# Optimization experiments

Measured on AMD Instinct MI355X. Metric: run time of the kernel, lower is better.

## Reference

```python
import jax, jax.numpy as jnp
import numpy as np
import math

NUM_HEADS = 16
HEAD_DIM = 128
ROPE_BASE = 10000.0


def setup_inputs() -> dict:
    key = jax.random.key(0)
    ks = jax.random.split(key, 6)
    B, S, H = 2, 2048, 2048
    hidden_states = jax.random.normal(ks[0], (B, S, H), dtype=jnp.float32) * 0.02
    # causal additive mask, shape (B, 1, S, S)
    neg = jnp.finfo(jnp.float32).min
    causal = jnp.where(jnp.tril(jnp.ones((S, S), dtype=bool)), 0.0, neg).astype(jnp.float32)
    attention_mask = jnp.broadcast_to(causal[None, None], (B, 1, S, S))
    position_ids = jnp.broadcast_to(jnp.arange(S, dtype=jnp.int64)[None], (B, S))
    scale = 1.0 / math.sqrt(H)
    Wq = jax.random.normal(ks[1], (H, H), dtype=jnp.float32) * scale
    Wk = jax.random.normal(ks[2], (H, H), dtype=jnp.float32) * scale
    Wv = jax.random.normal(ks[3], (H, H), dtype=jnp.float32) * scale
    Wo = jax.random.normal(ks[4], (H, H), dtype=jnp.float32) * scale
    return {"hidden_states": hidden_states, "attention_mask": attention_mask,
            "position_ids": position_ids, "Wq": Wq, "Wk": Wk, "Wv": Wv, "Wo": Wo}


def _rotate_half(x):
    x1, x2 = jnp.split(x, 2, axis=-1)
    return jnp.concatenate((-x2, x1), axis=-1)


def reference(hidden_states, attention_mask, position_ids, Wq, Wk, Wv, Wo):
    B, S, H = hidden_states.shape
    nh, hd = NUM_HEADS, HEAD_DIM

    def shape_heads(x):  # (B,S,H) -> (B,nh,S,hd)
        return x.reshape(B, S, nh, hd).transpose(0, 2, 1, 3)

    q = shape_heads(hidden_states @ Wq.T)
    k = shape_heads(hidden_states @ Wk.T)
    v = shape_heads(hidden_states @ Wv.T)

    kv_seq_len = S  # no past_key_value
    # rotary table: (kv_seq_len, hd)
    inv_freq = 1.0 / (ROPE_BASE ** (jnp.arange(0, hd, 2, dtype=jnp.float32) / hd))
    t = jnp.arange(kv_seq_len, dtype=jnp.float32)
    freqs = jnp.einsum('i,j->ij', t, inv_freq)
    emb = jnp.concatenate((freqs, freqs), axis=-1)
    # gather-based RoPE == table lookup at position_ids: (B,S,hd) -> (B,1,S,hd)
    cos = jnp.cos(emb)[position_ids][:, None]
    sin = jnp.sin(emb)[position_ids][:, None]

    q = q * cos + _rotate_half(q) * sin
    k = k * cos + _rotate_half(k) * sin

    scores = jnp.einsum('bhqd,bhkd->bhqk', q, k) / math.sqrt(hd)
    scores = scores + attention_mask
    scores = jnp.maximum(scores, jnp.finfo(scores.dtype).min)
    probs = jax.nn.softmax(scores.astype(jnp.float32), axis=-1).astype(q.dtype)
    attn = jnp.einsum('bhqk,bhkd->bhqd', probs, v)  # (B,nh,S,hd)
    attn = attn.transpose(0, 2, 1, 3).reshape(B, S, H)
    return attn @ Wo.T
```

## Files before the change

kernel.cpp:

```cpp
#include <hip/hip_runtime.h>
#include <hip/hip_bf16.h>
#include <cstdint>

#define SQ    2048
#define HDIM  2048
#define NH    16
#define HD    128
#define BATCH 2
#define MTOK  (BATCH*SQ)

typedef unsigned short u16;
typedef unsigned int   u32;
typedef __bf16 bf16x8 __attribute__((ext_vector_type(8)));
typedef float  f32x4  __attribute__((ext_vector_type(4)));
typedef float  f32x16 __attribute__((ext_vector_type(16)));
typedef unsigned short u16x4 __attribute__((ext_vector_type(4)));
typedef unsigned int   u32x4 __attribute__((ext_vector_type(4)));

__device__ __forceinline__ u16 f2b(float f) {
  union { float f; unsigned u; } v; v.f = f;
  return (u16)((v.u + 0x7fffu + ((v.u >> 16) & 1u)) >> 16);
}
__device__ __forceinline__ float b2f(u16 b) {
  union { unsigned u; float f; } v; v.u = ((unsigned)b) << 16;
  return v.f;
}

#define GLD_LDS16(gp, lp) __builtin_amdgcn_global_load_lds( \
    (const __attribute__((address_space(1))) uint32_t*)(gp), \
    (__attribute__((address_space(3))) uint32_t*)(lp), 16, 0, 0)

__device__ __forceinline__ f32x16 zero16() {
  f32x16 v;
#pragma unroll
  for (int i = 0; i < 16; ++i) v[i] = 0.f;
  return v;
}

__global__ __launch_bounds__(256) void conv_bf16(const float* __restrict__ in,
                                                 u16* __restrict__ out, int n4) {
  int i = blockIdx.x * 256 + threadIdx.x;
  if (i >= n4) return;
  float4 v = ((const float4*)in)[i];
  u16x4 o;
  o.x = f2b(v.x); o.y = f2b(v.y); o.z = f2b(v.z); o.w = f2b(v.w);
  *(u16x4*)(out + (size_t)i * 4) = o;
}

__global__ void rope_table_k(float* __restrict__ ct, float* __restrict__ st) {
  int s = blockIdx.x, j = threadIdx.x;
  float invf = expf(-(float)j * (9.210340371976184f / 64.0f));
  float ang = (float)s * invf;
  ct[s * 64 + j] = cosf(ang);
  st[s * 64 + j] = sinf(ang);
}

__global__ __launch_bounds__(256) void rope_apply(u16* __restrict__ X,
                                                  const float* __restrict__ ct,
                                                  const float* __restrict__ st) {
  int idx = blockIdx.x * 256 + threadIdx.x;
  int j = idx & 63;
  int row = idx >> 6;
  int s = row & (SQ - 1);
  size_t base = (size_t)row * HD;
  float x1 = b2f(X[base + j]), x2 = b2f(X[base + j + 64]);
  float c = ct[s * 64 + j], sn = st[s * 64 + j];
  X[base + j]      = f2b(x1 * c - x2 * sn);
  X[base + j + 64] = f2b(x2 * c + x1 * sn);
}

template<int MODE>
__global__ __launch_bounds__(256)
void gemm_bt(const u16* __restrict__ A, const u16* __restrict__ Bw,
             void* __restrict__ Cout) {
  __shared__ u16 As[128 * 64];
  __shared__ u16 Bs[128 * 64];
  const int tid = threadIdx.x;
  const int lane = tid & 63;
  const int w = tid >> 6;
  const int m0 = blockIdx.y * 128;
  const int n0 = blockIdx.x * 128;
  const int wm = (w >> 1) * 64;
  const int wn = (w & 1) * 64;
  const int lr = lane >> 3, lc = lane & 7;

  f32x4 zero = {0.f, 0.f, 0.f, 0.f};
  f32x4 acc[4][4];
  for (int i = 0; i < 4; ++i)
    for (int j = 0; j < 4; ++j) acc[i][j] = zero;

  for (int k0 = 0; k0 < HDIM; k0 += 64) {
    __syncthreads();
#pragma unroll
    for (int j = 0; j < 4; ++j) {
      int r = (w * 4 + j) * 8 + lr;
      GLD_LDS16(A  + (size_t)(m0 + r) * HDIM + k0 + lc * 8, &As[(w * 4 + j) * 512]);
      GLD_LDS16(Bw + (size_t)(n0 + r) * HDIM + k0 + lc * 8, &Bs[(w * 4 + j) * 512]);
    }
    __syncthreads();
#pragma unroll
    for (int kk = 0; kk < 2; ++kk) {
      int ko = kk * 32 + (lane >> 4) * 8;
      bf16x8 a[4], b[4];
#pragma unroll
      for (int i = 0; i < 4; ++i)
        a[i] = *(const bf16x8*)&As[(wm + i * 16 + (lane & 15)) * 64 + ko];
#pragma unroll
      for (int i = 0; i < 4; ++i)
        b[i] = *(const bf16x8*)&Bs[(wn + i * 16 + (lane & 15)) * 64 + ko];
#pragma unroll
      for (int mi = 0; mi < 4; ++mi)
#pragma unroll
        for (int ni = 0; ni < 4; ++ni)
          acc[mi][ni] = __builtin_amdgcn_mfma_f32_16x16x32_bf16(
              a[mi], b[ni], acc[mi][ni], 0, 0, 0);
    }
  }

  const int cl = lane & 15, rg = (lane >> 4) * 4;
#pragma unroll
  for (int mi = 0; mi < 4; ++mi) {
#pragma unroll
    for (int ni = 0; ni < 4; ++ni) {
      int mbase = m0 + wm + mi * 16 + rg;
      int n = n0 + wn + ni * 16 + cl;
      if (MODE == 2) {
        float* O = (float*)Cout;
#pragma unroll
        for (int r = 0; r < 4; ++r)
          O[(size_t)(mbase + r) * HDIM + n] = acc[mi][ni][r];
      } else if (MODE == 0) {
        u16* O = (u16*)Cout;
        int h = n >> 7, d = n & 127;
#pragma unroll
        for (int r = 0; r < 4; ++r) {
          int m = mbase + r;
          int b = m >> 11, s = m & (SQ - 1);
          O[((size_t)(b * NH + h) * SQ + s) * HD + d] = f2b(acc[mi][ni][r]);
        }
      } else {
        u16* O = (u16*)Cout;
        int h = n >> 7, d = n & 127;
        int b = mbase >> 11, s = mbase & (SQ - 1);
        u16x4 pk;
        pk.x = f2b(acc[mi][ni][0]); pk.y = f2b(acc[mi][ni][1]);
        pk.z = f2b(acc[mi][ni][2]); pk.w = f2b(acc[mi][ni][3]);
        *(u16x4*)&O[((size_t)(b * NH + h) * HD + d) * SQ + s] = pk;
      }
    }
  }
}


__device__ __forceinline__ void stage_kv(u16* ksb, u16* vsb,
                                         const u16* __restrict__ Kg,
                                         const u16* __restrict__ Vg,
                                         int kv0, int w, int lane) {
#pragma unroll
  for (int i = 0; i < 4; ++i) {
    int chunk = (w * 4 + i) * 64 + lane;
    int row = chunk >> 4, c16 = chunk & 15;
    int csrc = c16 ^ (row & 7);
    GLD_LDS16(Kg + (size_t)(kv0 + row) * HD + csrc * 8, ksb + (w * 4 + i) * 512);
  }
#pragma unroll
  for (int i = 0; i < 4; ++i) {
    int chunk = (w * 4 + i) * 64 + lane;
    int d = chunk >> 3, c8 = chunk & 7;
    int csrc = c8 ^ (d & 7);
    GLD_LDS16(Vg + (size_t)d * SQ + kv0 + csrc * 8, vsb + (w * 4 + i) * 512);
  }
}

#define MKPA(dst, P, off) { \
  u32 u0_, u1_, u2_, u3_; \
  asm("v_cvt_pk_bf16_f32 %0, %1, %2" : "=v"(u0_) : "v"(P[off + 0]), "v"(P[off + 1])); \
  asm("v_cvt_pk_bf16_f32 %0, %1, %2" : "=v"(u1_) : "v"(P[off + 2]), "v"(P[off + 3])); \
  asm("v_cvt_pk_bf16_f32 %0, %1, %2" : "=v"(u2_) : "v"(P[off + 4]), "v"(P[off + 5])); \
  asm("v_cvt_pk_bf16_f32 %0, %1, %2" : "=v"(u3_) : "v"(P[off + 6]), "v"(P[off + 7])); \
  u32 x0_ = (u32)__shfl_xor((int)u0_, 32, 64); \
  u32 x1_ = (u32)__shfl_xor((int)u1_, 32, 64); \
  u32 x2_ = (u32)__shfl_xor((int)u2_, 32, 64); \
  u32 x3_ = (u32)__shfl_xor((int)u3_, 32, 64); \
  u32x4 w_; \
  w_.x = hi ? x2_ : u0_; \
  w_.y = hi ? x3_ : u1_; \
  w_.z = hi ? u2_ : x0_; \
  w_.w = hi ? u3_ : x1_; \
  dst = __builtin_bit_cast(bf16x8, w_); \
}

#define PVD(oD, dblk) { \
  const int dr_ = (dblk) * 32 + l31; \
  const int sw_ = (dr_ & 7) << 4; \
  bf16x8 v0_ = *(const bf16x8*)(Vb + ((dr_ * 128 +  0 + hi * 16) ^ sw_)); \
  oD = __builtin_amdgcn_mfma_f32_32x32x16_bf16(pa[0], v0_, oD, 0, 0, 0); \
  bf16x8 v1_ = *(const bf16x8*)(Vb + ((dr_ * 128 + 32 + hi * 16) ^ sw_)); \
  oD = __builtin_amdgcn_mfma_f32_32x32x16_bf16(pa[1], v1_, oD, 0, 0, 0); \
  bf16x8 v2_ = *(const bf16x8*)(Vb + ((dr_ * 128 + 64 + hi * 16) ^ sw_)); \
  oD = __builtin_amdgcn_mfma_f32_32x32x16_bf16(pa[2], v2_, oD, 0, 0, 0); \
  bf16x8 v3_ = *(const bf16x8*)(Vb + ((dr_ * 128 + 96 + hi * 16) ^ sw_)); \
  oD = __builtin_amdgcn_mfma_f32_32x32x16_bf16(pa[3], v3_, oD, 0, 0, 0); \
}

__global__ __launch_bounds__(256, 2)
void flash_fwd2(const u16* __restrict__ Q, const u16* __restrict__ K,
                const u16* __restrict__ Vt, u16* __restrict__ Out) {
  __shared__ u16 Ks[2][64 * 128];
  __shared__ u16 Vs[2][128 * 64];
  const int tid = threadIdx.x, lane = tid & 63, w = tid >> 6;
  const int hi = lane >> 5, l31 = lane & 31;
  const int qt = 15 - (int)(blockIdx.x >> 5);
  const int bh = blockIdx.x & 31;
  const int q0 = qt * 128;
  const u16* Qg = Q + (size_t)bh * SQ * HD;
  const u16* Kg = K + (size_t)bh * SQ * HD;
  const u16* Vg = Vt + (size_t)bh * HD * SQ;
  const int qw = q0 + w * 32;
  const int qg = qw + l31;

  bf16x8 qf[8];
#pragma unroll
  for (int st = 0; st < 8; ++st)
    qf[st] = *(const bf16x8*)&Qg[(size_t)qg * HD + st * 16 + hi * 8];

  f32x16 o0 = zero16(), o1 = zero16(), o2 = zero16(), o3 = zero16();
  float lsum = 0.f;
  const float sL2E = 0.1275174446f;
  const int ktl = 2 * qt + 1;
  int cur = 0;

  stage_kv(Ks[0], Vs[0], Kg, Vg, 0, w, lane);

  for (int kt = 0; kt <= ktl; ++kt) {
    if (kt < ktl) {
      stage_kv(Ks[cur ^ 1], Vs[cur ^ 1], Kg, Vg, (kt + 1) * 64, w, lane);
      asm volatile("s_waitcnt vmcnt(8)" ::: "memory");
    } else {
      asm volatile("s_waitcnt vmcnt(0)" ::: "memory");
    }
    __builtin_amdgcn_s_barrier();

    const int kv0 = kt * 64;
    if (kv0 <= qw + 31) {
      const char* Kb = (const char*)Ks[cur];
      const char* Vb = (const char*)Vs[cur];
      f32x16 c0 = zero16(), c1 = zero16();
      const int kr0 = l31, kr1 = 32 + l31;
      const int sw0 = (kr0 & 7) << 4;
#pragma unroll
      for (int st = 0; st < 8; ++st) {
        bf16x8 k0 = *(const bf16x8*)(Kb + ((kr0 * 256 + st * 32 + hi * 16) ^ sw0));
        c0 = __builtin_amdgcn_mfma_f32_32x32x16_bf16(k0, qf[st], c0, 0, 0, 0);
        bf16x8 k1 = *(const bf16x8*)(Kb + ((kr1 * 256 + st * 32 + hi * 16) ^ sw0));
        c1 = __builtin_amdgcn_mfma_f32_32x32x16_bf16(k1, qf[st], c1, 0, 0, 0);
      }
      const bool needmask = (kv0 + 63 > qw);
      const int lim0 = qg - kv0, lim1 = lim0 - 32;
      if (needmask) {
#pragma unroll
        for (int r = 0; r < 16; ++r) {
          const int cr = (r & 3) + 8 * (r >> 2) + 4 * hi;
          float p0 = exp2f(c0[r] * sL2E);
          c0[r] = (cr <= lim0) ? p0 : 0.f;
          float p1 = exp2f(c1[r] * sL2E);
          c1[r] = (cr <= lim1) ? p1 : 0.f;
          lsum += c0[r] + c1[r];
        }
      } else {
#pragma unroll
        for (int r = 0; r < 16; ++r) {
          c0[r] = exp2f(c0[r] * sL2E);
          c1[r] = exp2f(c1[r] * sL2E);
          lsum += c0[r] + c1[r];
        }
      }
      bf16x8 pa[4];
      MKPA(pa[0], c0, 0); MKPA(pa[1], c0, 8);
      MKPA(pa[2], c1, 0); MKPA(pa[3], c1, 8);
      PVD(o0, 0) PVD(o1, 1) PVD(o2, 2) PVD(o3, 3)
    }
    __builtin_amdgcn_s_barrier();
    cur ^= 1;
  }

  float ltot = lsum + __shfl_xor(lsum, 32, 64);
  float invl = 1.f / ltot;
  const int b = bh >> 4, h = bh & 15;
#pragma unroll
  for (int g = 0; g < 4; ++g) {
#pragma unroll
    for (int j = 0; j < 4; ++j) {
      const int r = g * 4 + j;
      const int cr = g * 8 + 4 * hi + j;
      float inv = __shfl(invl, cr, 64);
      const int s = q0 + w * 32 + cr;
      size_t rb = ((size_t)(b * SQ + s)) * HDIM + h * HD;
      Out[rb +  0 + l31] = f2b(o0[r] * inv);
      Out[rb + 32 + l31] = f2b(o1[r] * inv);
      Out[rb + 64 + l31] = f2b(o2[r] * inv);
      Out[rb + 96 + l31] = f2b(o3[r] * inv);
    }
  }
}

extern "C" void kernel_launch(void* const* d_in, const int* in_sizes, int n_in,
                              void* d_out, int out_size, void* d_ws, size_t ws_size,
                              hipStream_t stream) {
  const float* hs = (const float*)d_in[0];
  const float* Wq = (const float*)d_in[3];
  const float* Wk = (const float*)d_in[4];
  const float* Wv = (const float*)d_in[5];
  const float* Wo = (const float*)d_in[6];

  char* ws = (char*)d_ws;
  u16* XB  = (u16*)(ws);
  u16* WQB = (u16*)(ws + (size_t)(16 << 20));
  u16* WKB = (u16*)(ws + (size_t)(24 << 20));
  u16* WVB = (u16*)(ws + (size_t)(32 << 20));
  u16* WOB = (u16*)(ws + (size_t)(40 << 20));
  u16* QR  = (u16*)(ws + (size_t)(48 << 20));
  u16* KR  = (u16*)(ws + (size_t)(64 << 20));
  u16* VT  = (u16*)(ws + (size_t)(80 << 20));
  u16* ATT = (u16*)(ws + (size_t)(96 << 20));
  float* CT = (float*)(ws + (size_t)(112 << 20));
  float* ST = (float*)(ws + (size_t)(112 << 20) + (1 << 19));

  conv_bf16<<<8192, 256, 0, stream>>>(hs, XB, 2097152);
  conv_bf16<<<4096, 256, 0, stream>>>(Wq, WQB, 1048576);
  conv_bf16<<<4096, 256, 0, stream>>>(Wk, WKB, 1048576);
  conv_bf16<<<4096, 256, 0, stream>>>(Wv, WVB, 1048576);
  conv_bf16<<<4096, 256, 0, stream>>>(Wo, WOB, 1048576);
  rope_table_k<<<SQ, 64, 0, stream>>>(CT, ST);

  dim3 ggrid(HDIM / 128, MTOK / 128);
  gemm_bt<0><<<ggrid, 256, 0, stream>>>(XB, WQB, QR);
  gemm_bt<0><<<ggrid, 256, 0, stream>>>(XB, WKB, KR);
  gemm_bt<1><<<ggrid, 256, 0, stream>>>(XB, WVB, VT);

  rope_apply<<<16384, 256, 0, stream>>>(QR, CT, ST);
  rope_apply<<<16384, 256, 0, stream>>>(KR, CT, ST);

  flash_fwd2<<<512, 256, 0, stream>>>(QR, KR, VT, ATT);

  gemm_bt<2><<<ggrid, 256, 0, stream>>>(ATT, WOB, d_out);
}
```

Before: 314.2 us.

## Replace GEMMs with double-buffered 256x256 tile kernel and batch small launches

Swaps the 128x128 single-buffered GEMM for a 512-thread, 256x256-tile kernel with LDS double buffering, XOR-swizzled LDS layout, and raised wave priority around the MFMA blocks. The Q/K/V projections become one launch, and the weight conversions and both RoPE applications are each merged into one launch. Priority hints are also added to the flash-attention MFMA sections. The aim is more reuse per tile, overlap of loads with math, and fewer launches. The trade-off is heavy LDS use (128 KB per block), which limits occupancy, and the output projection runs only 128 blocks, which may underfill the GPU.

```diff
diff --git a/kernel.cpp b/kernel.cpp
--- a/kernel.cpp
+++ b/kernel.cpp
@@ -47,6 +47,21 @@
   *(u16x4*)(out + (size_t)i * 4) = o;
 }
 
+__global__ __launch_bounds__(256) void conv_w4(const float* __restrict__ w0,
+                                               const float* __restrict__ w1,
+                                               const float* __restrict__ w2,
+                                               const float* __restrict__ w3,
+                                               u16* o0, u16* o1, u16* o2, u16* o3) {
+  int i = blockIdx.x * 256 + threadIdx.x;
+  int sel = blockIdx.y;
+  const float* in = sel == 0 ? w0 : sel == 1 ? w1 : sel == 2 ? w2 : w3;
+  u16* out = sel == 0 ? o0 : sel == 1 ? o1 : sel == 2 ? o2 : o3;
+  float4 v = ((const float4*)in)[i];
+  u16x4 o;
+  o.x = f2b(v.x); o.y = f2b(v.y); o.z = f2b(v.z); o.w = f2b(v.w);
+  *(u16x4*)(out + (size_t)i * 4) = o;
+}
+
 __global__ void rope_table_k(float* __restrict__ ct, float* __restrict__ st) {
   int s = blockIdx.x, j = threadIdx.x;
   float invf = expf(-(float)j * (9.210340371976184f / 64.0f));
@@ -55,9 +70,11 @@
   st[s * 64 + j] = sinf(ang);
 }
 
-__global__ __launch_bounds__(256) void rope_apply(u16* __restrict__ X,
-                                                  const float* __restrict__ ct,
-                                                  const float* __restrict__ st) {
+__global__ __launch_bounds__(256) void rope_apply2(u16* __restrict__ Xq,
+                                                   u16* __restrict__ Xk,
+                                                   const float* __restrict__ ct,
+                                                   const float* __restrict__ st) {
+  u16* X = blockIdx.y ? Xk : Xq;
   int idx = blockIdx.x * 256 + threadIdx.x;
   int j = idx & 63;
   int row = idx >> 6;
@@ -69,83 +86,131 @@
   X[base + j + 64] = f2b(x2 * c + x1 * sn);
 }
 
-template<int MODE>
-__global__ __launch_bounds__(256)
-void gemm_bt(const u16* __restrict__ A, const u16* __restrict__ Bw,
-             void* __restrict__ Cout) {
-  __shared__ u16 As[128 * 64];
-  __shared__ u16 Bs[128 * 64];
-  const int tid = threadIdx.x;
-  const int lane = tid & 63;
-  const int w = tid >> 6;
-  const int m0 = blockIdx.y * 128;
-  const int n0 = blockIdx.x * 128;
-  const int wm = (w >> 1) * 64;
-  const int wn = (w & 1) * 64;
-  const int lr = lane >> 3, lc = lane & 7;
-
-  f32x4 zero = {0.f, 0.f, 0.f, 0.f};
-  f32x4 acc[4][4];
-  for (int i = 0; i < 4; ++i)
-    for (int j = 0; j < 4; ++j) acc[i][j] = zero;
-
-  for (int k0 = 0; k0 < HDIM; k0 += 64) {
-    __syncthreads();
-#pragma unroll
-    for (int j = 0; j < 4; ++j) {
-      int r = (w * 4 + j) * 8 + lr;
-      GLD_LDS16(A  + (size_t)(m0 + r) * HDIM + k0 + lc * 8, &As[(w * 4 + j) * 512]);
-      GLD_LDS16(Bw + (size_t)(n0 + r) * HDIM + k0 + lc * 8, &Bs[(w * 4 + j) * 512]);
-    }
-    __syncthreads();
-#pragma unroll
-    for (int kk = 0; kk < 2; ++kk) {
-      int ko = kk * 32 + (lane >> 4) * 8;
-      bf16x8 a[4], b[4];
-#pragma unroll
-      for (int i = 0; i < 4; ++i)
-        a[i] = *(const bf16x8*)&As[(wm + i * 16 + (lane & 15)) * 64 + ko];
-#pragma unroll
-      for (int i = 0; i < 4; ++i)
-        b[i] = *(const bf16x8*)&Bs[(wn + i * 16 + (lane & 15)) * 64 + ko];
-#pragma unroll
-      for (int mi = 0; mi < 4; ++mi)
-#pragma unroll
-        for (int ni = 0; ni < 4; ++ni)
-          acc[mi][ni] = __builtin_amdgcn_mfma_f32_16x16x32_bf16(
-              a[mi], b[ni], acc[mi][ni], 0, 0, 0);
-    }
-  }
-
-  const int cl = lane & 15, rg = (lane >> 4) * 4;
-#pragma unroll
-  for (int mi = 0; mi < 4; ++mi) {
+template<int OUT>
+__global__ __launch_bounds__(512, 2)
+void gemm8(const u16* __restrict__ A, const u16* __restrict__ W0,
+           const u16* __restrict__ W1, const u16* __restrict__ W2,
+           u16* __restrict__ oQ, u16* __restrict__ oK, u16* __restrict__ oV,
+           float* __restrict__ oF) {
+  __shared__ u16 Asb[2][256 * 64];
+  __shared__ u16 Bsb[2][256 * 64];
+  const int tid = threadIdx.x, lane = tid & 63, w = tid >> 6;
+  const int wm = w >> 2, wn = w & 3;
+  const int m0 = blockIdx.y * 256;
+  const int n0g = blockIdx.x * 256;
+  int sel; const u16* Bw; int nloc;
+  if (OUT == 0) {
+    sel = n0g >> 11;
+    Bw = (sel == 0) ? W0 : (sel == 1) ? W1 : W2;
+    nloc = n0g & 2047;
+  } else {
+    sel = 0; Bw = W0; nloc = n0g;
+  }
+
+  size_t aoff[4], boff[4];
+  int ldso[4];
+#pragma unroll
+  for (int i = 0; i < 4; ++i) {
+    int c = i * 512 + tid;
+    int r = c >> 3, sl = c & 7;
+    aoff[i] = (size_t)(m0 + r) * HDIM + ((sl ^ (r & 7)) * 8);
+    boff[i] = (size_t)(nloc + r) * HDIM + ((sl ^ (r & 7)) * 8);
+    ldso[i] = (i * 512 + w * 64) * 8;
+  }
+
+  auto stage = [&](u16* As_, u16* Bs_, int k0_) {
+#pragma unroll
+    for (int i = 0; i < 4; ++i) {
+      GLD_LDS16(A + aoff[i] + k0_, As_ + ldso[i]);
+      GLD_LDS16(Bw + boff[i] + k0_, Bs_ + ldso[i]);
+    }
+  };
+
+  f32x4 acc[8][4];
+#pragma unroll
+  for (int i = 0; i < 8; ++i)
+#pragma unroll
+    for (int j = 0; j < 4; ++j) acc[i][j] = (f32x4){0.f, 0.f, 0.f, 0.f};
+
+  const int l15 = lane & 15, hi4 = lane >> 4;
+  const int swr = (l15 & 7) << 4;
+
+  stage((u16*)Asb[0], (u16*)Bsb[0], 0);
+
+  const int NT = HDIM / 64;
+  for (int t = 0; t < NT; ++t) {
+    const int cur = t & 1;
+    if (t + 1 < NT) {
+      stage((u16*)Asb[cur ^ 1], (u16*)Bsb[cur ^ 1], (t + 1) * 64);
+      asm volatile("s_waitcnt vmcnt(8)" ::: "memory");
+    } else {
+      asm volatile("s_waitcnt vmcnt(0)" ::: "memory");
+    }
+    __builtin_amdgcn_s_barrier();
+
+    const char* Ab = (const char*)(cur ? Asb[1] : Asb[0]);
+    const char* Bb = (const char*)(cur ? Bsb[1] : Bsb[0]);
+
+    bf16x8 bf[4][2];
+#pragma unroll
+    for (int ni = 0; ni < 4; ++ni)
+#pragma unroll
+      for (int kk = 0; kk < 2; ++kk)
+        bf[ni][kk] = *(const bf16x8*)(Bb + (wn * 64 + ni * 16 + l15) * 128 +
+                                      ((kk * 64 + hi4 * 16) ^ swr));
+#pragma unroll
+    for (int p = 0; p < 4; ++p) {
+      bf16x8 af[2][2];
+#pragma unroll
+      for (int j = 0; j < 2; ++j)
+#pragma unroll
+        for (int kk = 0; kk < 2; ++kk)
+          af[j][kk] = *(const bf16x8*)(Ab + (wm * 128 + (2 * p + j) * 16 + l15) * 128 +
+                                       ((kk * 64 + hi4 * 16) ^ swr));
+      __builtin_amdgcn_s_barrier();
+      asm volatile("s_waitcnt lgkmcnt(0)" ::: "memory");
+      __builtin_amdgcn_sched_barrier(0);
+      __builtin_amdgcn_s_setprio(1);
+#pragma unroll
+      for (int kk = 0; kk < 2; ++kk)
+#pragma unroll
+        for (int j = 0; j < 2; ++j)
+#pragma unroll
+          for (int ni = 0; ni < 4; ++ni)
+            acc[2 * p + j][ni] = __builtin_amdgcn_mfma_f32_16x16x32_bf16(
+                af[j][kk], bf[ni][kk], acc[2 * p + j][ni], 0, 0, 0);
+      __builtin_amdgcn_s_setprio(0);
+      __builtin_amdgcn_s_barrier();
+    }
+  }
+
+  const int cl = l15, rg = hi4 * 4;
+#pragma unroll
+  for (int mi = 0; mi < 8; ++mi) {
 #pragma unroll
     for (int ni = 0; ni < 4; ++ni) {
-      int mbase = m0 + wm + mi * 16 + rg;
-      int n = n0 + wn + ni * 16 + cl;
-      if (MODE == 2) {
-        float* O = (float*)Cout;
+      const int mb = m0 + wm * 128 + mi * 16 + rg;
+      const int n = nloc + wn * 64 + ni * 16 + cl;
+      if (OUT == 1) {
 #pragma unroll
         for (int r = 0; r < 4; ++r)
-          O[(size_t)(mbase + r) * HDIM + n] = acc[mi][ni][r];
-      } else if (MODE == 0) {
-        u16* O = (u16*)Cout;
-        int h = n >> 7, d = n & 127;
-#pragma unroll
-        for (int r = 0; r < 4; ++r) {
-          int m = mbase + r;
-          int b = m >> 11, s = m & (SQ - 1);
-          O[((size_t)(b * NH + h) * SQ + s) * HD + d] = f2b(acc[mi][ni][r]);
+          oF[(size_t)(mb + r) * HDIM + n] = acc[mi][ni][r];
+      } else {
+        const int h = n >> 7, d = n & 127;
+        if (sel == 2) {
+          const int b = mb >> 11, s = mb & (SQ - 1);
+          u16x4 pk;
+          pk.x = f2b(acc[mi][ni][0]); pk.y = f2b(acc[mi][ni][1]);
+          pk.z = f2b(acc[mi][ni][2]); pk.w = f2b(acc[mi][ni][3]);
+          *(u16x4*)&oV[((size_t)(b * NH + h) * HD + d) * SQ + s] = pk;
+        } else {
+          u16* O = sel ? oK : oQ;
+#pragma unroll
+          for (int r = 0; r < 4; ++r) {
+            const int m = mb + r, b = m >> 11, s = m & (SQ - 1);
+            O[((size_t)(b * NH + h) * SQ + s) * HD + d] = f2b(acc[mi][ni][r]);
+          }
         }
-      } else {
-        u16* O = (u16*)Cout;
-        int h = n >> 7, d = n & 127;
-        int b = mbase >> 11, s = mbase & (SQ - 1);
-        u16x4 pk;
-        pk.x = f2b(acc[mi][ni][0]); pk.y = f2b(acc[mi][ni][1]);
-        pk.z = f2b(acc[mi][ni][2]); pk.w = f2b(acc[mi][ni][3]);
-        *(u16x4*)&O[((size_t)(b * NH + h) * HD + d) * SQ + s] = pk;
       }
     }
   }
@@ -248,6 +313,7 @@
       f32x16 c0 = zero16(), c1 = zero16();
       const int kr0 = l31, kr1 = 32 + l31;
       const int sw0 = (kr0 & 7) << 4;
+      __builtin_amdgcn_s_setprio(1);
 #pragma unroll
       for (int st = 0; st < 8; ++st) {
         bf16x8 k0 = *(const bf16x8*)(Kb + ((kr0 * 256 + st * 32 + hi * 16) ^ sw0));
@@ -255,6 +321,7 @@
         bf16x8 k1 = *(const bf16x8*)(Kb + ((kr1 * 256 + st * 32 + hi * 16) ^ sw0));
         c1 = __builtin_amdgcn_mfma_f32_32x32x16_bf16(k1, qf[st], c1, 0, 0, 0);
       }
+      __builtin_amdgcn_s_setprio(0);
       const bool needmask = (kv0 + 63 > qw);
       const int lim0 = qg - kv0, lim1 = lim0 - 32;
       if (needmask) {
@@ -278,7 +345,9 @@
       bf16x8 pa[4];
       MKPA(pa[0], c0, 0); MKPA(pa[1], c0, 8);
       MKPA(pa[2], c1, 0); MKPA(pa[3], c1, 8);
+      __builtin_amdgcn_s_setprio(1);
       PVD(o0, 0) PVD(o1, 1) PVD(o2, 2) PVD(o3, 3)
+      __builtin_amdgcn_s_setprio(0);
     }
     __builtin_amdgcn_s_barrier();
     cur ^= 1;
@@ -327,21 +396,15 @@
   float* ST = (float*)(ws + (size_t)(112 << 20) + (1 << 19));
 
   conv_bf16<<<8192, 256, 0, stream>>>(hs, XB, 2097152);
-  conv_bf16<<<4096, 256, 0, stream>>>(Wq, WQB, 1048576);
-  conv_bf16<<<4096, 256, 0, stream>>>(Wk, WKB, 1048576);
-  conv_bf16<<<4096, 256, 0, stream>>>(Wv, WVB, 1048576);
-  conv_bf16<<<4096, 256, 0, stream>>>(Wo, WOB, 1048576);
+  conv_w4<<<dim3(4096, 4), 256, 0, stream>>>(Wq, Wk, Wv, Wo, WQB, WKB, WVB, WOB);
   rope_table_k<<<SQ, 64, 0, stream>>>(CT, ST);
 
-  dim3 ggrid(HDIM / 128, MTOK / 128);
-  gemm_bt<0><<<ggrid, 256, 0, stream>>>(XB, WQB, QR);
-  gemm_bt<0><<<ggrid, 256, 0, stream>>>(XB, WKB, KR);
-  gemm_bt<1><<<ggrid, 256, 0, stream>>>(XB, WVB, VT);
-
-  rope_apply<<<16384, 256, 0, stream>>>(QR, CT, ST);
-  rope_apply<<<16384, 256, 0, stream>>>(KR, CT, ST);
+  gemm8<0><<<dim3(24, 16), 512, 0, stream>>>(XB, WQB, WKB, WVB, QR, KR, VT, nullptr);
+
+  rope_apply2<<<dim3(16384, 2), 256, 0, stream>>>(QR, KR, CT, ST);
 
   flash_fwd2<<<512, 256, 0, stream>>>(QR, KR, VT, ATT);
 
-  gemm_bt<2><<<ggrid, 256, 0, stream>>>(ATT, WOB, d_out);
-}
+  gemm8<1><<<dim3(8, 16), 512, 0, stream>>>(ATT, WOB, nullptr, nullptr,
+                                            nullptr, nullptr, nullptr, (float*)d_out);
+}
```

After: 341.3 us. 1.09x slower.
